# Kernel tuning notes

Measured on AMD Instinct MI355X. Metric: run time of the kernel, lower is better.

The kernel has to match this reference:

```python
import jax, jax.numpy as jnp
import numpy as np

PATCH_LENS = [8, 16, 24, 48]
MAX_P = 48
MIN_P = 8
TARGET = MAX_P // MIN_P  # 6 patches per region after repeat_interleave
N_EXP = len(PATCH_LENS)
D_MODEL = 512
TAU = 0.5


def _repeat_idx(plen):
    # Mirrors: patches.repeat_interleave(repeat+1, dim=1)[:, :TARGET]
    n = MAX_P // plen
    k = TARGET - n + 1  # repeat + 1
    idx = np.arange(TARGET) // k if k > 1 else np.arange(TARGET)
    return jnp.asarray(np.minimum(idx, n - 1), dtype=jnp.int32)


def _pos_emb(L, d):
    # PositionalEmbedding buffer (sin/cos), sliced to length L
    pos = np.arange(L, dtype=np.float64)[:, None]
    div = np.exp(np.arange(0, d, 2, dtype=np.float64) * -(np.log(10000.0) / d))
    pe = np.zeros((L, d), np.float32)
    pe[:, 0::2] = np.sin(pos * div).astype(np.float32)
    pe[:, 1::2] = np.cos(pos * div).astype(np.float32)
    return jnp.asarray(pe)


def setup_inputs() -> dict:
    key = jax.random.key(0)
    ks = jax.random.split(key, 8)
    B, C, S = 128, 32, 336
    N, R = B * C, S // MAX_P
    x = jax.random.normal(ks[0], (B, C, S), dtype=jnp.float32)
    u_noise = jax.random.uniform(ks[1], (N, R, N_EXP), dtype=jnp.float32)
    W1 = jax.random.normal(ks[2], (MAX_P, 64), dtype=jnp.float32) * 0.02
    b1 = jnp.zeros((64,), jnp.float32)
    W2 = jax.random.normal(ks[3], (64, N_EXP), dtype=jnp.float32) * 0.02
    b2 = jnp.zeros((N_EXP,), jnp.float32)
    W_emb0 = jax.random.normal(ks[4], (PATCH_LENS[0], D_MODEL), dtype=jnp.float32) * 0.02
    W_emb1 = jax.random.normal(ks[5], (PATCH_LENS[1], D_MODEL), dtype=jnp.float32) * 0.02
    W_emb2 = jax.random.normal(ks[6], (PATCH_LENS[2], D_MODEL), dtype=jnp.float32) * 0.02
    W_emb3 = jax.random.normal(ks[7], (PATCH_LENS[3], D_MODEL), dtype=jnp.float32) * 0.02
    return {"x": x, "u_noise": u_noise, "W1": W1, "b1": b1, "W2": W2, "b2": b2,
            "W_emb0": W_emb0, "W_emb1": W_emb1, "W_emb2": W_emb2, "W_emb3": W_emb3}


def reference(x, u_noise, W1, b1, W2, b2, W_emb0, W_emb1, W_emb2, W_emb3):
    B, C, S = x.shape
    R = S // MAX_P
    xr = x.reshape(B * C, R, MAX_P)                       # [N, R, 48]

    # Region-wise router MLP (vectorized over all regions)
    logits = jax.nn.relu(xr @ W1 + b1) @ W2 + b2          # [N, R, E]
    # Gumbel-softmax (tau=0.5, hard=True, straight-through)
    g = -jnp.log(-jnp.log(u_noise + 1e-10) + 1e-10)
    soft = jax.nn.softmax((logits + g) / TAU, axis=-1)
    hard = jax.nn.one_hot(jnp.argmax(soft, axis=-1), N_EXP, dtype=soft.dtype)
    cls_soft = hard + soft - jax.lax.stop_gradient(soft)  # [N, R, E]

    # Per-candidate-patch-length embedding, weighted combine (accumulate to cap memory)
    W_embs = [W_emb0, W_emb1, W_emb2, W_emb3]
    out = jnp.zeros((B * C, R, TARGET, D_MODEL), dtype=x.dtype)
    for i, plen in enumerate(PATCH_LENS):
        n = MAX_P // plen
        # unfold(step==size) == reshape; then repeat_interleave+slice == static gather
        patches = xr.reshape(B * C, R, n, plen)[:, :, _repeat_idx(plen), :]  # [N,R,T,plen]
        emb = patches @ W_embs[i]                          # [N, R, T, d]
        out = out + emb * cls_soft[..., i][..., None, None]

    x_patch = out.reshape(B * C, R * TARGET, D_MODEL)
    x_patch = x_patch + _pos_emb(R * TARGET, D_MODEL)[None]

    # torch.cat of per-region [N] argmaxes along dim 0 -> region-major flatten
    cls_pred = jnp.argmax(cls_soft, axis=-1).T.reshape(-1)  # [R*N]
    return x_patch, jnp.int32(C), cls_pred
```

## Files before the change

### kernel.cpp

```cpp
#include <hip/hip_runtime.h>
#include <math.h>


namespace {
constexpr int NROWS = 4096;
constexpr int SEQ   = 336;
constexpr int RREG  = 7;
constexpr int TGT   = 6;
constexpr int DM    = 512;
constexpr int DM4   = DM / 4;
constexpr int NEXP  = 4;
constexpr long long XP_ELEMS = (long long)NROWS * RREG * TGT * DM;
constexpr int PE_ELEMS = RREG * TGT * DM;
}

typedef float v4f __attribute__((ext_vector_type(4)));

__global__ void pe_kernel(float* __restrict__ pe) {
    int i = blockIdx.x * blockDim.x + threadIdx.x;
    if (i >= PE_ELEMS) return;
    int p = i / DM, d = i - p * DM;
    int j = d >> 1;
    double div = exp((double)(2 * j) * -(log(10000.0) / (double)DM));
    double a = (double)p * div;
    pe[i] = (d & 1) ? (float)cos(a) : (float)sin(a);
}

__device__ inline float pe_val(int p, int d) {
    int j = d >> 1;
    float div = __expf((float)(2 * j) * (-9.210340371976184f / 512.0f));
    float a = (float)p * div;
    return (d & 1) ? __cosf(a) : __sinf(a);
}

template <bool HAVE_PE>
__global__ __launch_bounds__(256) void apk_kernel(
    const float* __restrict__ x,   const float* __restrict__ un,
    const float* __restrict__ W1,  const float* __restrict__ b1,
    const float* __restrict__ W2,  const float* __restrict__ b2,
    const float* __restrict__ We0, const float* __restrict__ We1,
    const float* __restrict__ We2, const float* __restrict__ We3,
    const float* __restrict__ pe,  float* __restrict__ out)
{
    const int blk = blockIdx.x;
    const int n = blk / RREG;
    const int r = blk - n * RREG;
    const int tid = threadIdx.x;

    __shared__ float sx[48];
    __shared__ float sh[64];
    __shared__ float sz[NEXP];
    __shared__ float s_w;
    __shared__ int   s_e;

    if (tid < 48) sx[tid] = x[(size_t)n * SEQ + r * 48 + tid];
    __syncthreads();

    if (tid < 64) {
        float h = b1[tid];
        #pragma unroll
        for (int k = 0; k < 48; ++k) h = fmaf(sx[k], W1[k * 64 + tid], h);
        sh[tid] = fmaxf(h, 0.0f);
    }
    __syncthreads();

    if (tid < NEXP) {
        float z = b2[tid];
        #pragma unroll
        for (int j = 0; j < 64; ++j) z = fmaf(sh[j], W2[j * NEXP + tid], z);
        float uu = un[(size_t)blk * NEXP + tid];
        float g = -logf(-logf(uu + 1e-10f) + 1e-10f);
        sz[tid] = (z + g) / 0.5f;
    }
    __syncthreads();

    if (tid == 0) {
        float z0 = sz[0], z1 = sz[1], z2 = sz[2], z3 = sz[3];
        int e = 0; float zm = z0;
        if (z1 > zm) { zm = z1; e = 1; }
        if (z2 > zm) { zm = z2; e = 2; }
        if (z3 > zm) { zm = z3; e = 3; }
        float s = 1.0f / (((expf(z0 - zm) + expf(z1 - zm)) + expf(z2 - zm)) + expf(z3 - zm));
        s_e = e;
        s_w = (1.0f + s) - s;
        out[(size_t)XP_ELEMS + 1 + (size_t)r * NROWS + n] = (float)e;
        if (blk == 0) out[(size_t)XP_ELEMS] = 32.0f;
    }
    __syncthreads();

    const int e = s_e;
    const float w = s_w;
    const int c4   = tid & 127;
    const int half = tid >> 7;
    v4f* __restrict__ outv = reinterpret_cast<v4f*>(out);
    const v4f* __restrict__ pev = reinterpret_cast<const v4f*>(pe);
    const size_t ob = ((size_t)n * (RREG * TGT) + (size_t)r * TGT) * DM4;
    const int pb = r * TGT * DM4;

    auto pe4 = [&](int t) -> v4f {
        if constexpr (HAVE_PE) {
            return pev[pb + t * DM4 + c4];
        } else {
            v4f v;
            v.x = pe_val(r * TGT + t, 4 * c4 + 0);
            v.y = pe_val(r * TGT + t, 4 * c4 + 1);
            v.z = pe_val(r * TGT + t, 4 * c4 + 2);
            v.w = pe_val(r * TGT + t, 4 * c4 + 3);
            return v;
        }
    };
    auto emit = [&](int t, const v4f& a) {
        v4f pv = pe4(t);
        v4f v;
        v.x = fmaf(a.x, w, pv.x);
        v.y = fmaf(a.y, w, pv.y);
        v.z = fmaf(a.z, w, pv.z);
        v.w = fmaf(a.w, w, pv.w);
        __builtin_nontemporal_store(v, &outv[ob + (size_t)t * DM4 + c4]);
    };
    auto fma4 = [](float xv, const v4f& wv, v4f& a) {
        a.x = fmaf(xv, wv.x, a.x);
        a.y = fmaf(xv, wv.y, a.y);
        a.z = fmaf(xv, wv.z, a.z);
        a.w = fmaf(xv, wv.w, a.w);
    };
    const v4f zero4 = (v4f)(0.0f);

    if (e == 0) {
        const v4f* W = reinterpret_cast<const v4f*>(We0);
        v4f a0 = zero4, a1 = zero4, a2 = zero4;
        #pragma unroll
        for (int k = 0; k < 8; ++k) {
            v4f wv = W[k * DM4 + c4];
            fma4(sx[(half + 0) * 8 + k], wv, a0);
            fma4(sx[(half + 2) * 8 + k], wv, a1);
            fma4(sx[(half + 4) * 8 + k], wv, a2);
        }
        emit(half + 0, a0);
        emit(half + 2, a1);
        emit(half + 4, a2);
    } else if (e == 1) {
        const v4f* W = reinterpret_cast<const v4f*>(We1);
        v4f a0 = zero4, a1 = zero4;
        #pragma unroll
        for (int k = 0; k < 16; ++k) {
            v4f wv = W[k * DM4 + c4];
            fma4(sx[k],      wv, a0);
            fma4(sx[16 + k], wv, a1);
        }
        #pragma unroll
        for (int i = 0; i < 3; ++i) {
            int t = half + 2 * i;
            emit(t, (t < 4) ? a0 : a1);
        }
    } else if (e == 2) {
        const v4f* W = reinterpret_cast<const v4f*>(We2);
        v4f a0 = zero4, a1 = zero4;
        #pragma unroll
        for (int k = 0; k < 24; ++k) {
            v4f wv = W[k * DM4 + c4];
            fma4(sx[k],      wv, a0);
            fma4(sx[24 + k], wv, a1);
        }
        #pragma unroll
        for (int i = 0; i < 3; ++i) {
            int t = half + 2 * i;
            emit(t, (t < 5) ? a0 : a1);
        }
    } else {
        const v4f* W = reinterpret_cast<const v4f*>(We3);
        v4f a0 = zero4;
        #pragma unroll
        for (int k = 0; k < 48; ++k) {
            v4f wv = W[k * DM4 + c4];
            fma4(sx[k], wv, a0);
        }
        #pragma unroll
        for (int i = 0; i < 3; ++i) emit(half + 2 * i, a0);
    }
}

extern "C" void kernel_launch(void* const* d_in, const int* in_sizes, int n_in,
                              void* d_out, int out_size, void* d_ws, size_t ws_size,
                              hipStream_t stream) {
    const float* x   = (const float*)d_in[0];
    const float* un  = (const float*)d_in[1];
    const float* W1  = (const float*)d_in[2];
    const float* b1  = (const float*)d_in[3];
    const float* W2  = (const float*)d_in[4];
    const float* b2  = (const float*)d_in[5];
    const float* We0 = (const float*)d_in[6];
    const float* We1 = (const float*)d_in[7];
    const float* We2 = (const float*)d_in[8];
    const float* We3 = (const float*)d_in[9];
    float* out = (float*)d_out;

    const int nblk = NROWS * RREG;
    const bool have_pe = ws_size >= (size_t)PE_ELEMS * sizeof(float);

    if (have_pe) {
        float* pe = (float*)d_ws;
        pe_kernel<<<(PE_ELEMS + 255) / 256, 256, 0, stream>>>(pe);
        apk_kernel<true><<<nblk, 256, 0, stream>>>(
            x, un, W1, b1, W2, b2, We0, We1, We2, We3, pe, out);
    } else {
        apk_kernel<false><<<nblk, 256, 0, stream>>>(
            x, un, W1, b1, W2, b2, We0, We1, We2, We3, (const float*)nullptr, out);
    }
}
```

Baseline: 462.1 us.

## Split router MLP into separate thread-per-region kernel before embedding kernel

```diff
diff --git a/kernel.cpp b/kernel.cpp
--- a/kernel.cpp
+++ b/kernel.cpp
@@ -10,11 +10,14 @@
 constexpr int DM    = 512;
 constexpr int DM4   = DM / 4;
 constexpr int NEXP  = 4;
+constexpr int NREG  = NROWS * RREG;
 constexpr long long XP_ELEMS = (long long)NROWS * RREG * TGT * DM;
 constexpr int PE_ELEMS = RREG * TGT * DM;
+constexpr size_t WS_FLOATS = (size_t)PE_ELEMS + (size_t)NREG * 2;
 }
 
 typedef float v4f __attribute__((ext_vector_type(4)));
+typedef float v2f __attribute__((ext_vector_type(2)));
 
 __global__ void pe_kernel(float* __restrict__ pe) {
     int i = blockIdx.x * blockDim.x + threadIdx.x;
@@ -33,11 +36,58 @@
     return (d & 1) ? __cosf(a) : __sinf(a);
 }
 
-template <bool HAVE_PE>
-__global__ __launch_bounds__(256) void apk_kernel(
-    const float* __restrict__ x,   const float* __restrict__ un,
-    const float* __restrict__ W1,  const float* __restrict__ b1,
-    const float* __restrict__ W2,  const float* __restrict__ b2,
+__global__ __launch_bounds__(256) void router_kernel(
+    const float* __restrict__ x,  const float* __restrict__ un,
+    const float* __restrict__ W1, const float* __restrict__ b1,
+    const float* __restrict__ W2, const float* __restrict__ b2,
+    v2f* __restrict__ ew, float* __restrict__ out)
+{
+    const int g = blockIdx.x * 256 + threadIdx.x;
+    if (g >= NREG) return;
+    const int n = g / RREG, r = g - n * RREG;
+
+    float xv[48];
+    const v4f* xr4 = reinterpret_cast<const v4f*>(x + (size_t)n * SEQ + r * 48);
+    #pragma unroll
+    for (int i = 0; i < 12; ++i) {
+        v4f v = xr4[i];
+        xv[4 * i + 0] = v.x; xv[4 * i + 1] = v.y;
+        xv[4 * i + 2] = v.z; xv[4 * i + 3] = v.w;
+    }
+
+    float z0 = b2[0], z1 = b2[1], z2 = b2[2], z3 = b2[3];
+    for (int j = 0; j < 64; ++j) {
+        float h = b1[j];
+        #pragma unroll
+        for (int k = 0; k < 48; ++k) h = fmaf(xv[k], W1[k * 64 + j], h);
+        h = fmaxf(h, 0.0f);
+        z0 = fmaf(h, W2[j * NEXP + 0], z0);
+        z1 = fmaf(h, W2[j * NEXP + 1], z1);
+        z2 = fmaf(h, W2[j * NEXP + 2], z2);
+        z3 = fmaf(h, W2[j * NEXP + 3], z3);
+    }
+
+    const float* ug = un + (size_t)g * NEXP;
+    z0 = (z0 + -logf(-logf(ug[0] + 1e-10f) + 1e-10f)) / 0.5f;
+    z1 = (z1 + -logf(-logf(ug[1] + 1e-10f) + 1e-10f)) / 0.5f;
+    z2 = (z2 + -logf(-logf(ug[2] + 1e-10f) + 1e-10f)) / 0.5f;
+    z3 = (z3 + -logf(-logf(ug[3] + 1e-10f) + 1e-10f)) / 0.5f;
+
+    int e = 0; float zm = z0;
+    if (z1 > zm) { zm = z1; e = 1; }
+    if (z2 > zm) { zm = z2; e = 2; }
+    if (z3 > zm) { zm = z3; e = 3; }
+    float s = 1.0f / (((expf(z0 - zm) + expf(z1 - zm)) + expf(z2 - zm)) + expf(z3 - zm));
+    float w = (1.0f + s) - s;
+
+    v2f p; p.x = w; p.y = (float)e;
+    ew[g] = p;
+    out[(size_t)XP_ELEMS + 1 + (size_t)r * NROWS + n] = (float)e;
+    if (g == 0) out[(size_t)XP_ELEMS] = 32.0f;
+}
+
+__global__ __launch_bounds__(256) void embed_kernel(
+    const float* __restrict__ x,   const v2f* __restrict__ ew,
     const float* __restrict__ We0, const float* __restrict__ We1,
     const float* __restrict__ We2, const float* __restrict__ We3,
     const float* __restrict__ pe,  float* __restrict__ out)
@@ -47,6 +97,102 @@
     const int r = blk - n * RREG;
     const int tid = threadIdx.x;
 
+    const v2f ewv = ew[blk];
+    const float w = ewv.x;
+    const int e = (int)ewv.y;
+    const float* __restrict__ xr = x + (size_t)n * SEQ + r * 48;
+
+    const int c4   = tid & 127;
+    const int half = tid >> 7;
+    v4f* __restrict__ outv = reinterpret_cast<v4f*>(out);
+    const v4f* __restrict__ pev = reinterpret_cast<const v4f*>(pe);
+    const size_t ob = ((size_t)n * (RREG * TGT) + (size_t)r * TGT) * DM4;
+    const int pb = r * TGT * DM4;
+
+    auto emit = [&](int t, const v4f& a) {
+        v4f pv = pev[pb + t * DM4 + c4];
+        v4f v;
+        v.x = fmaf(a.x, w, pv.x);
+        v.y = fmaf(a.y, w, pv.y);
+        v.z = fmaf(a.z, w, pv.z);
+        v.w = fmaf(a.w, w, pv.w);
+        __builtin_nontemporal_store(v, &outv[ob + (size_t)t * DM4 + c4]);
+    };
+    auto fma4 = [](float xvv, const v4f& wv, v4f& a) {
+        a.x = fmaf(xvv, wv.x, a.x);
+        a.y = fmaf(xvv, wv.y, a.y);
+        a.z = fmaf(xvv, wv.z, a.z);
+        a.w = fmaf(xvv, wv.w, a.w);
+    };
+    const v4f zero4 = (v4f)(0.0f);
+
+    if (e == 0) {
+        const v4f* W = reinterpret_cast<const v4f*>(We0);
+        v4f a0 = zero4, a1 = zero4, a2 = zero4;
+        #pragma unroll
+        for (int k = 0; k < 8; ++k) {
+            v4f wv = W[k * DM4 + c4];
+            fma4(xr[(half + 0) * 8 + k], wv, a0);
+            fma4(xr[(half + 2) * 8 + k], wv, a1);
+            fma4(xr[(half + 4) * 8 + k], wv, a2);
+        }
+        emit(half + 0, a0);
+        emit(half + 2, a1);
+        emit(half + 4, a2);
+    } else if (e == 1) {
+        const v4f* W = reinterpret_cast<const v4f*>(We1);
+        v4f a0 = zero4, a1 = zero4;
+        #pragma unroll
+        for (int k = 0; k < 16; ++k) {
+            v4f wv = W[k * DM4 + c4];
+            fma4(xr[k],      wv, a0);
+            fma4(xr[16 + k], wv, a1);
+        }
+        #pragma unroll
+        for (int i = 0; i < 3; ++i) {
+            int t = half + 2 * i;
+            emit(t, (t < 4) ? a0 : a1);
+        }
+    } else if (e == 2) {
+        const v4f* W = reinterpret_cast<const v4f*>(We2);
+        v4f a0 = zero4, a1 = zero4;
+        #pragma unroll
+        for (int k = 0; k < 24; ++k) {
+            v4f wv = W[k * DM4 + c4];
+            fma4(xr[k],      wv, a0);
+            fma4(xr[24 + k], wv, a1);
+        }
+        #pragma unroll
+        for (int i = 0; i < 3; ++i) {
+            int t = half + 2 * i;
+            emit(t, (t < 5) ? a0 : a1);
+        }
+    } else {
+        const v4f* W = reinterpret_cast<const v4f*>(We3);
+        v4f a0 = zero4;
+        #pragma unroll
+        for (int k = 0; k < 48; ++k) {
+            v4f wv = W[k * DM4 + c4];
+            fma4(xr[k], wv, a0);
+        }
+        #pragma unroll
+        for (int i = 0; i < 3; ++i) emit(half + 2 * i, a0);
+    }
+}
+
+__global__ __launch_bounds__(256) void apk_fused_kernel(
+    const float* __restrict__ x,   const float* __restrict__ un,
+    const float* __restrict__ W1,  const float* __restrict__ b1,
+    const float* __restrict__ W2,  const float* __restrict__ b2,
+    const float* __restrict__ We0, const float* __restrict__ We1,
+    const float* __restrict__ We2, const float* __restrict__ We3,
+    float* __restrict__ out)
+{
+    const int blk = blockIdx.x;
+    const int n = blk / RREG;
+    const int r = blk - n * RREG;
+    const int tid = threadIdx.x;
+
     __shared__ float sx[48];
     __shared__ float sh[64];
     __shared__ float sz[NEXP];
@@ -55,7 +201,6 @@
 
     if (tid < 48) sx[tid] = x[(size_t)n * SEQ + r * 48 + tid];
     __syncthreads();
-
     if (tid < 64) {
         float h = b1[tid];
         #pragma unroll
@@ -63,7 +208,6 @@
         sh[tid] = fmaxf(h, 0.0f);
     }
     __syncthreads();
-
     if (tid < NEXP) {
         float z = b2[tid];
         #pragma unroll
@@ -73,7 +217,6 @@
         sz[tid] = (z + g) / 0.5f;
     }
     __syncthreads();
-
     if (tid == 0) {
         float z0 = sz[0], z1 = sz[1], z2 = sz[2], z3 = sz[3];
         int e = 0; float zm = z0;
@@ -93,21 +236,15 @@
     const int c4   = tid & 127;
     const int half = tid >> 7;
     v4f* __restrict__ outv = reinterpret_cast<v4f*>(out);
-    const v4f* __restrict__ pev = reinterpret_cast<const v4f*>(pe);
     const size_t ob = ((size_t)n * (RREG * TGT) + (size_t)r * TGT) * DM4;
-    const int pb = r * TGT * DM4;
 
     auto pe4 = [&](int t) -> v4f {
-        if constexpr (HAVE_PE) {
-            return pev[pb + t * DM4 + c4];
-        } else {
-            v4f v;
-            v.x = pe_val(r * TGT + t, 4 * c4 + 0);
-            v.y = pe_val(r * TGT + t, 4 * c4 + 1);
-            v.z = pe_val(r * TGT + t, 4 * c4 + 2);
-            v.w = pe_val(r * TGT + t, 4 * c4 + 3);
-            return v;
-        }
+        v4f v;
+        v.x = pe_val(r * TGT + t, 4 * c4 + 0);
+        v.y = pe_val(r * TGT + t, 4 * c4 + 1);
+        v.z = pe_val(r * TGT + t, 4 * c4 + 2);
+        v.w = pe_val(r * TGT + t, 4 * c4 + 3);
+        return v;
     };
     auto emit = [&](int t, const v4f& a) {
         v4f pv = pe4(t);
@@ -136,45 +273,32 @@
             fma4(sx[(half + 2) * 8 + k], wv, a1);
             fma4(sx[(half + 4) * 8 + k], wv, a2);
         }
-        emit(half + 0, a0);
-        emit(half + 2, a1);
-        emit(half + 4, a2);
+        emit(half + 0, a0); emit(half + 2, a1); emit(half + 4, a2);
     } else if (e == 1) {
         const v4f* W = reinterpret_cast<const v4f*>(We1);
         v4f a0 = zero4, a1 = zero4;
         #pragma unroll
         for (int k = 0; k < 16; ++k) {
             v4f wv = W[k * DM4 + c4];
-            fma4(sx[k],      wv, a0);
-            fma4(sx[16 + k], wv, a1);
-        }
-        #pragma unroll
-        for (int i = 0; i < 3; ++i) {
-            int t = half + 2 * i;
-            emit(t, (t < 4) ? a0 : a1);
-        }
+            fma4(sx[k], wv, a0); fma4(sx[16 + k], wv, a1);
+        }
+        #pragma unroll
+        for (int i = 0; i < 3; ++i) { int t = half + 2 * i; emit(t, (t < 4) ? a0 : a1); }
     } else if (e == 2) {
         const v4f* W = reinterpret_cast<const v4f*>(We2);
         v4f a0 = zero4, a1 = zero4;
         #pragma unroll
         for (int k = 0; k < 24; ++k) {
             v4f wv = W[k * DM4 + c4];
-            fma4(sx[k],      wv, a0);
-            fma4(sx[24 + k], wv, a1);
-        }
-        #pragma unroll
-        for (int i = 0; i < 3; ++i) {
-            int t = half + 2 * i;
-            emit(t, (t < 5) ? a0 : a1);
-        }
+            fma4(sx[k], wv, a0); fma4(sx[24 + k], wv, a1);
+        }
+        #pragma unroll
+        for (int i = 0; i < 3; ++i) { int t = half + 2 * i; emit(t, (t < 5) ? a0 : a1); }
     } else {
         const v4f* W = reinterpret_cast<const v4f*>(We3);
         v4f a0 = zero4;
         #pragma unroll
-        for (int k = 0; k < 48; ++k) {
-            v4f wv = W[k * DM4 + c4];
-            fma4(sx[k], wv, a0);
-        }
+        for (int k = 0; k < 48; ++k) { v4f wv = W[k * DM4 + c4]; fma4(sx[k], wv, a0); }
         #pragma unroll
         for (int i = 0; i < 3; ++i) emit(half + 2 * i, a0);
     }
@@ -195,16 +319,16 @@
     const float* We3 = (const float*)d_in[9];
     float* out = (float*)d_out;
 
-    const int nblk = NROWS * RREG;
-    const bool have_pe = ws_size >= (size_t)PE_ELEMS * sizeof(float);
-
-    if (have_pe) {
+    if (ws_size >= WS_FLOATS * sizeof(float)) {
         float* pe = (float*)d_ws;
+        v2f* ew = reinterpret_cast<v2f*>((float*)d_ws + PE_ELEMS);
         pe_kernel<<<(PE_ELEMS + 255) / 256, 256, 0, stream>>>(pe);
-        apk_kernel<true><<<nblk, 256, 0, stream>>>(
-            x, un, W1, b1, W2, b2, We0, We1, We2, We3, pe, out);
+        router_kernel<<<(NREG + 255) / 256, 256, 0, stream>>>(
+            x, un, W1, b1, W2, b2, ew, out);
+        embed_kernel<<<NREG, 256, 0, stream>>>(
+            x, ew, We0, We1, We2, We3, pe, out);
     } else {
-        apk_kernel<false><<<nblk, 256, 0, stream>>>(
-            x, un, W1, b1, W2, b2, We0, We1, We2, We3, (const float*)nullptr, out);
-    }
-}
+        apk_fused_kernel<<<NREG, 256, 0, stream>>>(
+            x, un, W1, b1, W2, b2, We0, We1, We2, We3, out);
+    }
+}
```

After: 446.2 us. 3.5% less time.

## Process all seven regions of a row per block with wave-parallel router

Applied to the files above, without the earlier changes.

```diff
diff --git a/kernel.cpp b/kernel.cpp
--- a/kernel.cpp
+++ b/kernel.cpp
@@ -34,7 +34,7 @@
 }
 
 template <bool HAVE_PE>
-__global__ __launch_bounds__(256) void apk_kernel(
+__global__ __launch_bounds__(256) void fused_kernel(
     const float* __restrict__ x,   const float* __restrict__ un,
     const float* __restrict__ W1,  const float* __restrict__ b1,
     const float* __restrict__ W2,  const float* __restrict__ b2,
@@ -42,141 +42,154 @@
     const float* __restrict__ We2, const float* __restrict__ We3,
     const float* __restrict__ pe,  float* __restrict__ out)
 {
-    const int blk = blockIdx.x;
-    const int n = blk / RREG;
-    const int r = blk - n * RREG;
-    const int tid = threadIdx.x;
-
-    __shared__ float sx[48];
-    __shared__ float sh[64];
-    __shared__ float sz[NEXP];
-    __shared__ float s_w;
-    __shared__ int   s_e;
-
-    if (tid < 48) sx[tid] = x[(size_t)n * SEQ + r * 48 + tid];
+    const int n    = blockIdx.x;
+    const int tid  = threadIdx.x;
+    const int lane = tid & 63;
+    const int wave = tid >> 6;
+
+    __shared__ float s_x[SEQ];
+    __shared__ float s_w[RREG];
+    __shared__ int   s_e[RREG];
+
+    s_x[tid] = x[(size_t)n * SEQ + tid];
+    if (tid < SEQ - 256) s_x[256 + tid] = x[(size_t)n * SEQ + 256 + tid];
     __syncthreads();
 
-    if (tid < 64) {
-        float h = b1[tid];
-        #pragma unroll
-        for (int k = 0; k < 48; ++k) h = fmaf(sx[k], W1[k * 64 + tid], h);
-        sh[tid] = fmaxf(h, 0.0f);
+    #pragma unroll
+    for (int rr = 0; rr < 2; ++rr) {
+        const int r = wave * 2 + rr;
+        if (r < RREG) {
+            const float* sx = &s_x[r * 48];
+            float h = b1[lane];
+            #pragma unroll
+            for (int k = 0; k < 48; ++k) h = fmaf(sx[k], W1[k * 64 + lane], h);
+            h = fmaxf(h, 0.0f);
+            float p0 = h * W2[lane * NEXP + 0];
+            float p1 = h * W2[lane * NEXP + 1];
+            float p2 = h * W2[lane * NEXP + 2];
+            float p3 = h * W2[lane * NEXP + 3];
+            #pragma unroll
+            for (int m = 1; m < 64; m <<= 1) {
+                p0 += __shfl_xor(p0, m);
+                p1 += __shfl_xor(p1, m);
+                p2 += __shfl_xor(p2, m);
+                p3 += __shfl_xor(p3, m);
+            }
+            if (lane == 0) {
+                const int g = n * RREG + r;
+                const float* ug = un + (size_t)g * NEXP;
+                float z0 = (b2[0] + p0 + -logf(-logf(ug[0] + 1e-10f) + 1e-10f)) / 0.5f;
+                float z1 = (b2[1] + p1 + -logf(-logf(ug[1] + 1e-10f) + 1e-10f)) / 0.5f;
+                float z2 = (b2[2] + p2 + -logf(-logf(ug[2] + 1e-10f) + 1e-10f)) / 0.5f;
+                float z3 = (b2[3] + p3 + -logf(-logf(ug[3] + 1e-10f) + 1e-10f)) / 0.5f;
+                int e = 0; float zm = z0;
+                if (z1 > zm) { zm = z1; e = 1; }
+                if (z2 > zm) { zm = z2; e = 2; }
+                if (z3 > zm) { zm = z3; e = 3; }
+                float s = 1.0f /
+                    (((expf(z0 - zm) + expf(z1 - zm)) + expf(z2 - zm)) + expf(z3 - zm));
+                s_w[r] = (1.0f + s) - s;
+                s_e[r] = e;
+                out[(size_t)XP_ELEMS + 1 + (size_t)r * NROWS + n] = (float)e;
+            }
+        }
     }
+    if (n == 0 && tid == 0) out[(size_t)XP_ELEMS] = 32.0f;
     __syncthreads();
 
-    if (tid < NEXP) {
-        float z = b2[tid];
-        #pragma unroll
-        for (int j = 0; j < 64; ++j) z = fmaf(sh[j], W2[j * NEXP + tid], z);
-        float uu = un[(size_t)blk * NEXP + tid];
-        float g = -logf(-logf(uu + 1e-10f) + 1e-10f);
-        sz[tid] = (z + g) / 0.5f;
-    }
-    __syncthreads();
-
-    if (tid == 0) {
-        float z0 = sz[0], z1 = sz[1], z2 = sz[2], z3 = sz[3];
-        int e = 0; float zm = z0;
-        if (z1 > zm) { zm = z1; e = 1; }
-        if (z2 > zm) { zm = z2; e = 2; }
-        if (z3 > zm) { zm = z3; e = 3; }
-        float s = 1.0f / (((expf(z0 - zm) + expf(z1 - zm)) + expf(z2 - zm)) + expf(z3 - zm));
-        s_e = e;
-        s_w = (1.0f + s) - s;
-        out[(size_t)XP_ELEMS + 1 + (size_t)r * NROWS + n] = (float)e;
-        if (blk == 0) out[(size_t)XP_ELEMS] = 32.0f;
-    }
-    __syncthreads();
-
-    const int e = s_e;
-    const float w = s_w;
     const int c4   = tid & 127;
     const int half = tid >> 7;
     v4f* __restrict__ outv = reinterpret_cast<v4f*>(out);
     const v4f* __restrict__ pev = reinterpret_cast<const v4f*>(pe);
-    const size_t ob = ((size_t)n * (RREG * TGT) + (size_t)r * TGT) * DM4;
-    const int pb = r * TGT * DM4;
-
-    auto pe4 = [&](int t) -> v4f {
-        if constexpr (HAVE_PE) {
-            return pev[pb + t * DM4 + c4];
+
+    for (int r = 0; r < RREG; ++r) {
+        const float w = s_w[r];
+        const int   e = s_e[r];
+        const float* sx = &s_x[r * 48];
+        const size_t ob = ((size_t)n * (RREG * TGT) + (size_t)r * TGT) * DM4;
+        const int pb = r * TGT * DM4;
+
+        auto pe4 = [&](int t) -> v4f {
+            if constexpr (HAVE_PE) {
+                return pev[pb + t * DM4 + c4];
+            } else {
+                v4f v;
+                v.x = pe_val(r * TGT + t, 4 * c4 + 0);
+                v.y = pe_val(r * TGT + t, 4 * c4 + 1);
+                v.z = pe_val(r * TGT + t, 4 * c4 + 2);
+                v.w = pe_val(r * TGT + t, 4 * c4 + 3);
+                return v;
+            }
+        };
+        auto emit = [&](int t, const v4f& a) {
+            v4f pv = pe4(t);
+            v4f v;
+            v.x = fmaf(a.x, w, pv.x);
+            v.y = fmaf(a.y, w, pv.y);
+            v.z = fmaf(a.z, w, pv.z);
+            v.w = fmaf(a.w, w, pv.w);
+            outv[ob + (size_t)t * DM4 + c4] = v;
+        };
+        auto fma4 = [](float xv, const v4f& wv, v4f& a) {
+            a.x = fmaf(xv, wv.x, a.x);
+            a.y = fmaf(xv, wv.y, a.y);
+            a.z = fmaf(xv, wv.z, a.z);
+            a.w = fmaf(xv, wv.w, a.w);
+        };
+        const v4f zero4 = (v4f)(0.0f);
+
+        if (e == 0) {
+            const v4f* W = reinterpret_cast<const v4f*>(We0);
+            v4f a0 = zero4, a1 = zero4, a2 = zero4;
+            #pragma unroll
+            for (int k = 0; k < 8; ++k) {
+                v4f wv = W[k * DM4 + c4];
+                fma4(sx[(half + 0) * 8 + k], wv, a0);
+                fma4(sx[(half + 2) * 8 + k], wv, a1);
+                fma4(sx[(half + 4) * 8 + k], wv, a2);
+            }
+            emit(half + 0, a0);
+            emit(half + 2, a1);
+            emit(half + 4, a2);
+        } else if (e == 1) {
+            const v4f* W = reinterpret_cast<const v4f*>(We1);
+            v4f a0 = zero4, a1 = zero4;
+            #pragma unroll
+            for (int k = 0; k < 16; ++k) {
+                v4f wv = W[k * DM4 + c4];
+                fma4(sx[k],      wv, a0);
+                fma4(sx[16 + k], wv, a1);
+            }
+            #pragma unroll
+            for (int i = 0; i < 3; ++i) {
+                int t = half + 2 * i;
+                emit(t, (t < 4) ? a0 : a1);
+            }
+        } else if (e == 2) {
+            const v4f* W = reinterpret_cast<const v4f*>(We2);
+            v4f a0 = zero4, a1 = zero4;
+            #pragma unroll
+            for (int k = 0; k < 24; ++k) {
+                v4f wv = W[k * DM4 + c4];
+                fma4(sx[k],      wv, a0);
+                fma4(sx[24 + k], wv, a1);
+            }
+            #pragma unroll
+            for (int i = 0; i < 3; ++i) {
+                int t = half + 2 * i;
+                emit(t, (t < 5) ? a0 : a1);
+            }
         } else {
-            v4f v;
-            v.x = pe_val(r * TGT + t, 4 * c4 + 0);
-            v.y = pe_val(r * TGT + t, 4 * c4 + 1);
-            v.z = pe_val(r * TGT + t, 4 * c4 + 2);
-            v.w = pe_val(r * TGT + t, 4 * c4 + 3);
-            return v;
+            const v4f* W = reinterpret_cast<const v4f*>(We3);
+            v4f a0 = zero4;
+            #pragma unroll
+            for (int k = 0; k < 48; ++k) {
+                v4f wv = W[k * DM4 + c4];
+                fma4(sx[k], wv, a0);
+            }
+            #pragma unroll
+            for (int i = 0; i < 3; ++i) emit(half + 2 * i, a0);
         }
-    };
-    auto emit = [&](int t, const v4f& a) {
-        v4f pv = pe4(t);
-        v4f v;
-        v.x = fmaf(a.x, w, pv.x);
-        v.y = fmaf(a.y, w, pv.y);
-        v.z = fmaf(a.z, w, pv.z);
-        v.w = fmaf(a.w, w, pv.w);
-        __builtin_nontemporal_store(v, &outv[ob + (size_t)t * DM4 + c4]);
-    };
-    auto fma4 = [](float xv, const v4f& wv, v4f& a) {
-        a.x = fmaf(xv, wv.x, a.x);
-        a.y = fmaf(xv, wv.y, a.y);
-        a.z = fmaf(xv, wv.z, a.z);
-        a.w = fmaf(xv, wv.w, a.w);
-    };
-    const v4f zero4 = (v4f)(0.0f);
-
-    if (e == 0) {
-        const v4f* W = reinterpret_cast<const v4f*>(We0);
-        v4f a0 = zero4, a1 = zero4, a2 = zero4;
-        #pragma unroll
-        for (int k = 0; k < 8; ++k) {
-            v4f wv = W[k * DM4 + c4];
-            fma4(sx[(half + 0) * 8 + k], wv, a0);
-            fma4(sx[(half + 2) * 8 + k], wv, a1);
-            fma4(sx[(half + 4) * 8 + k], wv, a2);
-        }
-        emit(half + 0, a0);
-        emit(half + 2, a1);
-        emit(half + 4, a2);
-    } else if (e == 1) {
-        const v4f* W = reinterpret_cast<const v4f*>(We1);
-        v4f a0 = zero4, a1 = zero4;
-        #pragma unroll
-        for (int k = 0; k < 16; ++k) {
-            v4f wv = W[k * DM4 + c4];
-            fma4(sx[k],      wv, a0);
-            fma4(sx[16 + k], wv, a1);
-        }
-        #pragma unroll
-        for (int i = 0; i < 3; ++i) {
-            int t = half + 2 * i;
-            emit(t, (t < 4) ? a0 : a1);
-        }
-    } else if (e == 2) {
-        const v4f* W = reinterpret_cast<const v4f*>(We2);
-        v4f a0 = zero4, a1 = zero4;
-        #pragma unroll
-        for (int k = 0; k < 24; ++k) {
-            v4f wv = W[k * DM4 + c4];
-            fma4(sx[k],      wv, a0);
-            fma4(sx[24 + k], wv, a1);
-        }
-        #pragma unroll
-        for (int i = 0; i < 3; ++i) {
-            int t = half + 2 * i;
-            emit(t, (t < 5) ? a0 : a1);
-        }
-    } else {
-        const v4f* W = reinterpret_cast<const v4f*>(We3);
-        v4f a0 = zero4;
-        #pragma unroll
-        for (int k = 0; k < 48; ++k) {
-            v4f wv = W[k * DM4 + c4];
-            fma4(sx[k], wv, a0);
-        }
-        #pragma unroll
-        for (int i = 0; i < 3; ++i) emit(half + 2 * i, a0);
     }
 }
 
@@ -195,16 +208,13 @@
     const float* We3 = (const float*)d_in[9];
     float* out = (float*)d_out;
 
-    const int nblk = NROWS * RREG;
-    const bool have_pe = ws_size >= (size_t)PE_ELEMS * sizeof(float);
-
-    if (have_pe) {
+    if (ws_size >= (size_t)PE_ELEMS * sizeof(float)) {
         float* pe = (float*)d_ws;
         pe_kernel<<<(PE_ELEMS + 255) / 256, 256, 0, stream>>>(pe);
-        apk_kernel<true><<<nblk, 256, 0, stream>>>(
+        fused_kernel<true><<<NROWS, 256, 0, stream>>>(
             x, un, W1, b1, W2, b2, We0, We1, We2, We3, pe, out);
     } else {
-        apk_kernel<false><<<nblk, 256, 0, stream>>>(
+        fused_kernel<false><<<NROWS, 256, 0, stream>>>(
             x, un, W1, b1, W2, b2, We0, We1, We2, We3, (const float*)nullptr, out);
     }
 }
```

New measurement: 527.4 us. +14.1%, slower.
